# Optimization experiments

Measured on AMD Instinct MI355X. Metric: run time of the kernel, lower is better.

Reference implementation:

```python
import jax, jax.numpy as jnp
import numpy as np

B = 32768          # batch
M = 128            # m_spa, embedding dim
N_TAB = 26         # number of sparse tables
N_ROWS = 100000    # rows per table
LN_BOT = [13, 512, 256, 128]
LN_TOP = [479, 1024, 1024, 1]  # 479 = 128 + 27*26/2

# strictly-lower-triangle indices of the (1+N_TAB) x (1+N_TAB) interaction matrix,
# in the same row-major order as the torch list-comprehension.
_LI, _LJ = np.tril_indices(N_TAB + 1, k=-1)


def _mlp_params(key, ln):
    ws, bs = [], []
    for i in range(len(ln) - 1):
        n, m = ln[i], ln[i + 1]
        key, k1, k2 = jax.random.split(key, 3)
        ws.append(jax.random.normal(k1, (m, n), jnp.float32) * np.sqrt(2.0 / (m + n)))
        bs.append(jax.random.normal(k2, (m,), jnp.float32) * np.sqrt(1.0 / m))
    return ws, bs


def setup_inputs() -> dict:
    key = jax.random.key(0)
    kd, ki, ke, kb, kt = jax.random.split(key, 5)
    dense_x = jax.random.normal(kd, (B, LN_BOT[0]), jnp.float32)
    lS_i = jax.random.randint(ki, (N_TAB, B), 0, N_ROWS, dtype=jnp.int64)
    lS_o = jnp.tile(jnp.arange(B, dtype=jnp.int64), (N_TAB, 1))  # one index per bag
    bound = np.sqrt(1.0 / N_ROWS)
    emb_W = jax.random.uniform(ke, (N_TAB, N_ROWS, M), jnp.float32, -bound, bound)
    bw, bb = _mlp_params(kb, LN_BOT)
    tw, tb = _mlp_params(kt, LN_TOP)
    return {
        "dense_x": dense_x, "lS_i": lS_i, "lS_o": lS_o, "emb_W": emb_W,
        "bot_w0": bw[0], "bot_b0": bb[0], "bot_w1": bw[1], "bot_b1": bb[1],
        "bot_w2": bw[2], "bot_b2": bb[2],
        "top_w0": tw[0], "top_b0": tb[0], "top_w1": tw[1], "top_b1": tb[1],
        "top_w2": tw[2], "top_b2": tb[2],
    }


def _forward(dense_x, lS_i, emb_W,
             bot_w0, bot_b0, bot_w1, bot_b1, bot_w2, bot_b2,
             top_w0, top_b0, top_w1, top_b1, top_w2, top_b2):
    # bottom MLP (all ReLU, sigmoid_bot = -1)
    x = jax.nn.relu(dense_x @ bot_w0.T + bot_b0)
    x = jax.nn.relu(x @ bot_w1.T + bot_b1)
    x = jax.nn.relu(x @ bot_w2.T + bot_b2)                      # [B, M]
    # embedding lookups; offsets are arange(B) -> sum-pool of a single index == gather
    ly = jax.vmap(lambda W, idx: W[idx])(emb_W, lS_i)           # [N_TAB, B, M]
    # pairwise feature interaction
    T = jnp.concatenate([x[:, None, :], jnp.transpose(ly, (1, 0, 2))], axis=1)  # [B, 27, M]
    Z = jnp.einsum('bid,bjd->bij', T, T)                        # [B, 27, 27]
    Zflat = Z[:, _LI, _LJ]                                      # [B, 351]
    R = jnp.concatenate([x, Zflat], axis=1)                     # [B, 479]
    # top MLP (ReLU, ReLU, Sigmoid at layer index 2)
    z = jax.nn.relu(R @ top_w0.T + top_b0)
    z = jax.nn.relu(z @ top_w1.T + top_b1)
    p = jax.nn.sigmoid(z @ top_w2.T + top_b2)                   # [B, 1]
    return p  # loss_threshold == 0.0 -> no clamp


def reference(dense_x, lS_i, lS_o, emb_W,
              bot_w0, bot_b0, bot_w1, bot_b1, bot_w2, bot_b2,
              top_w0, top_b0, top_w1, top_b1, top_w2, top_b2):
    del lS_o  # offsets = arange(B): one index per bag, pooling is identity
    return _forward(dense_x, lS_i, emb_W,
                    bot_w0, bot_b0, bot_w1, bot_b1, bot_w2, bot_b2,
                    top_w0, top_b0, top_w1, top_b1, top_w2, top_b2)
```

## Files before the change

kernel.cpp:

```cpp
#include <hip/hip_runtime.h>

typedef unsigned short u16;
typedef unsigned int   u32;
typedef __attribute__((ext_vector_type(4))) float f32x4;
typedef __attribute__((ext_vector_type(8))) short bf16x8;

__device__ __forceinline__ u16 f2bf(float f) {
  u32 u = __float_as_uint(f);
  u = (u + 0x7FFFu + ((u >> 16) & 1u)) >> 16;
  return (u16)u;
}
__device__ __forceinline__ float bf2f(u16 h) {
  return __uint_as_float(((u32)h) << 16);
}

#define GLDS16(gptr, lptr)                                      \
  __builtin_amdgcn_global_load_lds(                             \
      (const __attribute__((address_space(1))) void*)(gptr),    \
      (__attribute__((address_space(3))) void*)(lptr), 16, 0, 0)

__global__ __launch_bounds__(256) void cvt_w(const float* __restrict__ src,
                                             u16* __restrict__ dst, int n) {
  int i = blockIdx.x * 256 + threadIdx.x;
  if (i < n) dst[i] = f2bf(src[i]);
}

__global__ __launch_bounds__(256) void cvt_w_pad(const float* __restrict__ src,
                                                 u16* __restrict__ dst,
                                                 int N, int Ksrc, int Kdst) {
  int i = blockIdx.x * 256 + threadIdx.x;
  if (i < N * Kdst) {
    int r = i / Kdst, k = i - r * Kdst;
    dst[i] = (k < Ksrc) ? f2bf(src[(size_t)r * Ksrc + k]) : (u16)0;
  }
}

__global__ __launch_bounds__(256) void bot0(const float* __restrict__ dense,
                                            const float* __restrict__ w0,
                                            const float* __restrict__ b0,
                                            u16* __restrict__ x1) {
  const int t = blockIdx.x * 256 + threadIdx.x;
  const int b = t >> 9, n = t & 511;
  const float* dr = dense + (size_t)b * 13;
  const float* wr = w0 + (size_t)n * 13;
  float s = b0[n];
#pragma unroll
  for (int k = 0; k < 13; ++k) s = fmaf(dr[k], wr[k], s);
  x1[t] = f2bf(fmaxf(s, 0.f));
}

__global__ __launch_bounds__(256) void gemm_bt_relu(
    const u16* __restrict__ A, const u16* __restrict__ W,
    const float* __restrict__ bias, u16* __restrict__ C,
    int M, int N, int K) {
  __shared__ u16 Al[128 * 32];
  __shared__ u16 Bl[128 * 32];
  const int tid = threadIdx.x;
  const int wave = tid >> 6, lane = tid & 63;
  const int ntn = N >> 7;
  const int bm = blockIdx.x / ntn, bn = blockIdx.x % ntn;
  const int wm = (wave >> 1) << 6, wn = (wave & 1) << 6;
  const int fr = lane & 15, fq = lane >> 4;

  const int srow = wave * 16 + (lane >> 2);
  const int scol = (lane & 3) * 8;
  const u16* ag0 = A + (size_t)(bm * 128 + srow) * K + scol;
  const u16* ag1 = ag0 + (size_t)64 * K;
  const u16* wg0 = W + (size_t)(bn * 128 + srow) * K + scol;
  const u16* wg1 = wg0 + (size_t)64 * K;
  u16* la0 = &Al[(wave * 16) * 32];
  u16* la1 = &Al[(64 + wave * 16) * 32];
  u16* lb0 = &Bl[(wave * 16) * 32];
  u16* lb1 = &Bl[(64 + wave * 16) * 32];

  f32x4 acc[4][4] = {};

  for (int kt = 0; kt < K; kt += 32) {
    __syncthreads();
    GLDS16(ag0 + kt, la0);
    GLDS16(ag1 + kt, la1);
    GLDS16(wg0 + kt, lb0);
    GLDS16(wg1 + kt, lb1);
    __syncthreads();
    bf16x8 af[4], bfv[4];
#pragma unroll
    for (int i = 0; i < 4; ++i) {
      af[i]  = *(const bf16x8*)&Al[(wm + i * 16 + fr) * 32 + fq * 8];
      bfv[i] = *(const bf16x8*)&Bl[(wn + i * 16 + fr) * 32 + fq * 8];
    }
#pragma unroll
    for (int i = 0; i < 4; ++i)
#pragma unroll
      for (int j = 0; j < 4; ++j)
        acc[i][j] = __builtin_amdgcn_mfma_f32_16x16x32_bf16(af[i], bfv[j],
                                                            acc[i][j], 0, 0, 0);
  }

  const int crow0 = bm * 128 + wm, ccol0 = bn * 128 + wn;
#pragma unroll
  for (int i = 0; i < 4; ++i) {
#pragma unroll
    for (int j = 0; j < 4; ++j) {
      const int col = ccol0 + j * 16 + fr;
      const float bv = bias[col];
#pragma unroll
      for (int rr = 0; rr < 4; ++rr) {
        const int row = crow0 + i * 16 + fq * 4 + rr;
        float v = acc[i][j][rr] + bv;
        v = fmaxf(v, 0.f);
        C[(size_t)row * N + col] = f2bf(v);
      }
    }
  }
}

__global__ __launch_bounds__(256) void interact(const float* __restrict__ emb,
                                                const int* __restrict__ lsi,
                                                const u16* __restrict__ x3,
                                                u16* __restrict__ R) {
  const int wave = threadIdx.x >> 6, lane = threadIdx.x & 63;
  const int b = blockIdx.x * 4 + wave;
  const int fr = lane & 15, fq = lane >> 4;
  const u16* x3b = x3 + (size_t)b * 128;
  u16* Rb = R + (size_t)b * 512;

  *(u32*)&Rb[lane * 2] = *(const u32*)&x3b[lane * 2];
  if (lane < 33) Rb[479 + lane] = 0;

  bf16x8 tf[2][4];
#pragma unroll
  for (int mi = 0; mi < 2; ++mi) {
    const int row = mi * 16 + fr;
    if (row == 0) {
#pragma unroll
      for (int ks = 0; ks < 4; ++ks)
        tf[mi][ks] = *(const bf16x8*)&x3b[ks * 32 + fq * 8];
    } else if (row <= 26) {
      const int idx = lsi[(size_t)(row - 1) * 32768 + b];
      const float* er = emb + ((size_t)(row - 1) * 100000 + (size_t)idx) * 128;
#pragma unroll
      for (int ks = 0; ks < 4; ++ks) {
        f32x4 u0 = *(const f32x4*)&er[ks * 32 + fq * 8];
        f32x4 u1 = *(const f32x4*)&er[ks * 32 + fq * 8 + 4];
        bf16x8 v;
#pragma unroll
        for (int j = 0; j < 4; ++j) {
          v[j] = (short)f2bf(u0[j]);
          v[j + 4] = (short)f2bf(u1[j]);
        }
        tf[mi][ks] = v;
      }
    } else {
      bf16x8 z = {0, 0, 0, 0, 0, 0, 0, 0};
#pragma unroll
      for (int ks = 0; ks < 4; ++ks) tf[mi][ks] = z;
    }
  }

  f32x4 acc[2][2] = {};
#pragma unroll
  for (int ks = 0; ks < 4; ++ks)
#pragma unroll
    for (int mi = 0; mi < 2; ++mi)
#pragma unroll
      for (int ni = 0; ni < 2; ++ni)
        acc[mi][ni] = __builtin_amdgcn_mfma_f32_16x16x32_bf16(
            tf[mi][ks], tf[ni][ks], acc[mi][ni], 0, 0, 0);

#pragma unroll
  for (int mi = 0; mi < 2; ++mi)
#pragma unroll
    for (int ni = 0; ni < 2; ++ni)
#pragma unroll
      for (int rr = 0; rr < 4; ++rr) {
        const int i = mi * 16 + fq * 4 + rr;
        const int j = ni * 16 + fr;
        if (i < 27 && j < i)
          Rb[128 + (i * (i - 1)) / 2 + j] = f2bf(acc[mi][ni][rr]);
      }
}

__global__ __launch_bounds__(256) void final_k(const u16* __restrict__ z2,
                                               const float* __restrict__ w,
                                               const float* __restrict__ b2,
                                               float* __restrict__ out) {
  const int wave = threadIdx.x >> 6, lane = threadIdx.x & 63;
  const int b = blockIdx.x * 4 + wave;
  const u16* zr = z2 + (size_t)b * 1024;
  bf16x8 v0 = *(const bf16x8*)&zr[lane * 16];
  bf16x8 v1 = *(const bf16x8*)&zr[lane * 16 + 8];
  float s = 0.f;
#pragma unroll
  for (int j = 0; j < 8; ++j) {
    s = fmaf(bf2f((u16)v0[j]), w[lane * 16 + j], s);
    s = fmaf(bf2f((u16)v1[j]), w[lane * 16 + 8 + j], s);
  }
#pragma unroll
  for (int off = 32; off > 0; off >>= 1) s += __shfl_down(s, off, 64);
  if (lane == 0) out[b] = 1.f / (1.f + expf(-(s + b2[0])));
}

extern "C" void kernel_launch(void* const* d_in, const int* in_sizes, int n_in,
                              void* d_out, int out_size, void* d_ws,
                              size_t ws_size, hipStream_t stream) {
  const float* dense = (const float*)d_in[0];
  const int*   lsi   = (const int*)d_in[1];
  const float* emb = (const float*)d_in[3];
  const float* bw0 = (const float*)d_in[4];
  const float* bb0 = (const float*)d_in[5];
  const float* bw1 = (const float*)d_in[6];
  const float* bb1 = (const float*)d_in[7];
  const float* bw2 = (const float*)d_in[8];
  const float* bb2 = (const float*)d_in[9];
  const float* tw0 = (const float*)d_in[10];
  const float* tb0 = (const float*)d_in[11];
  const float* tw1 = (const float*)d_in[12];
  const float* tb1 = (const float*)d_in[13];
  const float* tw2 = (const float*)d_in[14];
  const float* tb2 = (const float*)d_in[15];

  char* ws = (char*)d_ws;
  u16* W1B  = (u16*)ws; ws += (size_t)256 * 512 * 2;
  u16* W2B  = (u16*)ws; ws += (size_t)128 * 256 * 2;
  u16* TW0B = (u16*)ws; ws += (size_t)1024 * 512 * 2;
  u16* TW1B = (u16*)ws; ws += (size_t)1024 * 1024 * 2;
  u16* X3   = (u16*)ws; ws += (size_t)32768 * 128 * 2;
  u16* SA   = (u16*)ws; ws += (size_t)32768 * 1024 * 2;
  u16* SB   = (u16*)ws; ws += (size_t)32768 * 1024 * 2;

  cvt_w<<<512, 256, 0, stream>>>(bw1, W1B, 256 * 512);
  cvt_w<<<128, 256, 0, stream>>>(bw2, W2B, 128 * 256);
  cvt_w_pad<<<2048, 256, 0, stream>>>(tw0, TW0B, 1024, 479, 512);
  cvt_w<<<4096, 256, 0, stream>>>(tw1, TW1B, 1024 * 1024);

  bot0<<<65536, 256, 0, stream>>>(dense, bw0, bb0, SA);
  gemm_bt_relu<<<512, 256, 0, stream>>>(SA, W1B, bb1, SB, 32768, 256, 512);
  gemm_bt_relu<<<256, 256, 0, stream>>>(SB, W2B, bb2, X3, 32768, 128, 256);
  interact<<<8192, 256, 0, stream>>>(emb, lsi, X3, SA);
  gemm_bt_relu<<<2048, 256, 0, stream>>>(SA, TW0B, tb0, SB, 32768, 1024, 512);
  gemm_bt_relu<<<2048, 256, 0, stream>>>(SB, TW1B, tb1, SA, 32768, 1024, 1024);
  final_k<<<8192, 256, 0, stream>>>(SA, tw2, tb2, (float*)d_out);
}
```

Measured before the change: 381.0 us.

## Add pipelined 256x256 GEMM for top MLP and fuse final dot into epilogue

Replaces the two large top-MLP GEMMs with a new 512-thread 256x256-tile kernel. It double-buffers LDS tiles via direct global-to-LDS loads, interleaves MFMA quarters with staged loads, raises wave priority around the MFMA blocks, and uses an XCD-aware block swizzle. The last GEMM's epilogue now computes the final 1024->1 dot product through atomicAdd into a float buffer, followed by a small sigmoid kernel. This removes the write and re-read of the 32768x1024 bf16 activation, at the cost of atomics, a zeroing kernel and a non-deterministic summation order.

```diff
diff --git a/kernel.cpp b/kernel.cpp
--- a/kernel.cpp
+++ b/kernel.cpp
@@ -18,6 +18,18 @@
   __builtin_amdgcn_global_load_lds(                             \
       (const __attribute__((address_space(1))) void*)(gptr),    \
       (__attribute__((address_space(3))) void*)(lptr), 16, 0, 0)
+
+#define BARRIER                                                 \
+  do {                                                          \
+    asm volatile("" ::: "memory");                              \
+    __builtin_amdgcn_s_barrier();                               \
+    asm volatile("" ::: "memory");                              \
+  } while (0)
+#define WAITLGKM0 asm volatile("s_waitcnt lgkmcnt(0)" ::: "memory")
+#define WAITVM2   asm volatile("s_waitcnt vmcnt(2)" ::: "memory")
+#define WAITVM0   asm volatile("s_waitcnt vmcnt(0)" ::: "memory")
+#define PRIO1 __builtin_amdgcn_s_setprio(1)
+#define PRIO0 __builtin_amdgcn_s_setprio(0)
 
 __global__ __launch_bounds__(256) void cvt_w(const float* __restrict__ src,
                                              u16* __restrict__ dst, int n) {
@@ -114,6 +126,139 @@
   }
 }
 
+#define LDA4(dst, FB, BUFE)                                                    \
+  _Pragma("unroll") for (int f = 0; f < 4; ++f)                                \
+  _Pragma("unroll") for (int ks = 0; ks < 2; ++ks)                             \
+    dst[f][ks] = *(const bf16x8*)&lds[(BUFE) +                                 \
+        (wm * 128 + (FB) * 16 + f * 16 + fr) * 64 +                            \
+        ((ks * 4 + fq) ^ fr7) * 8];
+
+#define LDB2(dst, GB, BUFE)                                                    \
+  _Pragma("unroll") for (int g = 0; g < 2; ++g)                                \
+  _Pragma("unroll") for (int ks = 0; ks < 2; ++ks)                             \
+    dst[g][ks] = *(const bf16x8*)&lds[(BUFE) + 16384 +                         \
+        (wn * 64 + (GB) * 16 + g * 16 + fr) * 64 +                             \
+        ((ks * 4 + fq) ^ fr7) * 8];
+
+#define MFQ(FB, GB, va, vb)                                                    \
+  _Pragma("unroll") for (int f = 0; f < 4; ++f)                                \
+  _Pragma("unroll") for (int g = 0; g < 2; ++g)                                \
+  _Pragma("unroll") for (int ks = 0; ks < 2; ++ks)                             \
+    acc[(FB) + f][(GB) + g] = __builtin_amdgcn_mfma_f32_16x16x32_bf16(         \
+        va[f][ks], vb[g][ks], acc[(FB) + f][(GB) + g], 0, 0, 0);
+
+template <int FUSE>
+__global__ __launch_bounds__(512, 2) void gemm256(
+    const u16* __restrict__ Ap, const u16* __restrict__ Wp,
+    const float* __restrict__ bias, u16* __restrict__ C,
+    const float* __restrict__ w2, float* __restrict__ dotacc,
+    int N, int K) {
+  __shared__ u16 lds[65536];
+  const int tid = threadIdx.x;
+  const int wave = tid >> 6, lane = tid & 63;
+  const int wm = wave >> 2, wn = wave & 3;
+  const int fr = lane & 15, fq = lane >> 4, fr7 = fr & 7;
+  const int nkt = K >> 6, NP = nkt >> 1;
+
+  const int nwg = gridDim.x;
+  const int swz = (blockIdx.x & 7) * (nwg >> 3) + (blockIdx.x >> 3);
+  const int ntn = N >> 8;
+  const int bm = swz / ntn, bn = swz % ntn;
+
+  auto stageH = [&](int tile, int half) {
+    const int isB = half >> 1;
+    const int h128 = half & 1;
+    const u16* mat = isB ? Wp : Ap;
+    const int brow0 = (isB ? bn : bm) * 256 + h128 * 128;
+    u16* lb = lds + (tile & 1) * 32768 + isB * 16384 + h128 * 8192 + wave * 512;
+    const int sl = lane >> 3;
+    const int ch = (lane & 7) ^ sl;
+    const u16* g = mat + (size_t)(brow0 + wave * 8 + sl) * K + tile * 64 + ch * 8;
+    GLDS16(g, lb);
+    GLDS16(g + (size_t)64 * K, lb + 4096);
+  };
+
+  f32x4 acc[8][4] = {};
+
+  stageH(0, 0); stageH(0, 1); stageH(0, 2); stageH(0, 3);
+  stageH(1, 0);
+  WAITVM2;
+  BARRIER;
+
+  for (int p = 0; p < NP; ++p) {
+    const int todd = 2 * p + 1, t2 = 2 * p + 2, t3 = 2 * p + 3;
+    const bool last = (p == NP - 1);
+    bf16x8 va[4][2], vb0[2][2], vb1[2][2];
+
+    LDA4(va, 0, 0); LDB2(vb0, 0, 0);
+    stageH(todd, 1);
+    BARRIER; WAITLGKM0; PRIO1; MFQ(0, 0, va, vb0); PRIO0; BARRIER;
+    LDB2(vb1, 2, 0);
+    stageH(todd, 2);
+    BARRIER; WAITLGKM0; PRIO1; MFQ(0, 2, va, vb1); PRIO0; BARRIER;
+    LDA4(va, 4, 0);
+    stageH(todd, 3);
+    BARRIER; WAITLGKM0; PRIO1; MFQ(4, 0, va, vb0); PRIO0; BARRIER;
+    if (t2 < nkt) stageH(t2, 0);
+    BARRIER; PRIO1; MFQ(4, 2, va, vb1); PRIO0;
+    if (last) { WAITVM0; } else { WAITVM2; }
+    BARRIER;
+
+    LDA4(va, 0, 32768); LDB2(vb0, 0, 32768);
+    if (t2 < nkt) stageH(t2, 1);
+    BARRIER; WAITLGKM0; PRIO1; MFQ(0, 0, va, vb0); PRIO0; BARRIER;
+    LDB2(vb1, 2, 32768);
+    if (t2 < nkt) stageH(t2, 2);
+    BARRIER; WAITLGKM0; PRIO1; MFQ(0, 2, va, vb1); PRIO0; BARRIER;
+    LDA4(va, 4, 32768);
+    if (t2 < nkt) stageH(t2, 3);
+    BARRIER; WAITLGKM0; PRIO1; MFQ(4, 0, va, vb0); PRIO0; BARRIER;
+    if (t3 < nkt) stageH(t3, 0);
+    BARRIER; PRIO1; MFQ(4, 2, va, vb1); PRIO0;
+    if (!last) { WAITVM2; }
+    BARRIER;
+  }
+
+  const int r0 = bm * 256 + wm * 128;
+  const int c0 = bn * 256 + wn * 64;
+  if (FUSE) {
+    float bv[4], wv[4];
+#pragma unroll
+    for (int g = 0; g < 4; ++g) {
+      const int col = c0 + g * 16 + fr;
+      bv[g] = bias[col];
+      wv[g] = w2[col];
+    }
+#pragma unroll
+    for (int f = 0; f < 8; ++f) {
+#pragma unroll
+      for (int rr = 0; rr < 4; ++rr) {
+        float s = 0.f;
+#pragma unroll
+        for (int g = 0; g < 4; ++g)
+          s += fmaxf(acc[f][g][rr] + bv[g], 0.f) * wv[g];
+#pragma unroll
+        for (int off = 8; off >= 1; off >>= 1) s += __shfl_xor(s, off, 64);
+        if (fr == 0)
+          atomicAdd(&dotacc[r0 + f * 16 + fq * 4 + rr], s);
+      }
+    }
+  } else {
+#pragma unroll
+    for (int g = 0; g < 4; ++g) {
+      const int col = c0 + g * 16 + fr;
+      const float bvv = bias[col];
+#pragma unroll
+      for (int f = 0; f < 8; ++f)
+#pragma unroll
+        for (int rr = 0; rr < 4; ++rr) {
+          const int row = r0 + f * 16 + fq * 4 + rr;
+          C[(size_t)row * N + col] = f2bf(fmaxf(acc[f][g][rr] + bvv, 0.f));
+        }
+    }
+  }
+}
+
 __global__ __launch_bounds__(256) void interact(const float* __restrict__ emb,
                                                 const int* __restrict__ lsi,
                                                 const u16* __restrict__ x3,
@@ -180,24 +325,16 @@
       }
 }
 
-__global__ __launch_bounds__(256) void final_k(const u16* __restrict__ z2,
-                                               const float* __restrict__ w,
-                                               const float* __restrict__ b2,
-                                               float* __restrict__ out) {
-  const int wave = threadIdx.x >> 6, lane = threadIdx.x & 63;
-  const int b = blockIdx.x * 4 + wave;
-  const u16* zr = z2 + (size_t)b * 1024;
-  bf16x8 v0 = *(const bf16x8*)&zr[lane * 16];
-  bf16x8 v1 = *(const bf16x8*)&zr[lane * 16 + 8];
-  float s = 0.f;
-#pragma unroll
-  for (int j = 0; j < 8; ++j) {
-    s = fmaf(bf2f((u16)v0[j]), w[lane * 16 + j], s);
-    s = fmaf(bf2f((u16)v1[j]), w[lane * 16 + 8 + j], s);
-  }
-#pragma unroll
-  for (int off = 32; off > 0; off >>= 1) s += __shfl_down(s, off, 64);
-  if (lane == 0) out[b] = 1.f / (1.f + expf(-(s + b2[0])));
+__global__ __launch_bounds__(256) void zero_f(float* __restrict__ p, int n) {
+  int i = blockIdx.x * 256 + threadIdx.x;
+  if (i < n) p[i] = 0.f;
+}
+
+__global__ __launch_bounds__(256) void sig_k(const float* __restrict__ accv,
+                                             const float* __restrict__ b2,
+                                             float* __restrict__ out, int n) {
+  int i = blockIdx.x * 256 + threadIdx.x;
+  if (i < n) out[i] = 1.f / (1.f + expf(-(accv[i] + b2[0])));
 }
 
 extern "C" void kernel_launch(void* const* d_in, const int* in_sizes, int n_in,
@@ -224,6 +361,7 @@
   u16* W2B  = (u16*)ws; ws += (size_t)128 * 256 * 2;
   u16* TW0B = (u16*)ws; ws += (size_t)1024 * 512 * 2;
   u16* TW1B = (u16*)ws; ws += (size_t)1024 * 1024 * 2;
+  float* DOT = (float*)ws; ws += (size_t)32768 * 4;
   u16* X3   = (u16*)ws; ws += (size_t)32768 * 128 * 2;
   u16* SA   = (u16*)ws; ws += (size_t)32768 * 1024 * 2;
   u16* SB   = (u16*)ws; ws += (size_t)32768 * 1024 * 2;
@@ -232,12 +370,15 @@
   cvt_w<<<128, 256, 0, stream>>>(bw2, W2B, 128 * 256);
   cvt_w_pad<<<2048, 256, 0, stream>>>(tw0, TW0B, 1024, 479, 512);
   cvt_w<<<4096, 256, 0, stream>>>(tw1, TW1B, 1024 * 1024);
+  zero_f<<<128, 256, 0, stream>>>(DOT, 32768);
 
   bot0<<<65536, 256, 0, stream>>>(dense, bw0, bb0, SA);
   gemm_bt_relu<<<512, 256, 0, stream>>>(SA, W1B, bb1, SB, 32768, 256, 512);
   gemm_bt_relu<<<256, 256, 0, stream>>>(SB, W2B, bb2, X3, 32768, 128, 256);
   interact<<<8192, 256, 0, stream>>>(emb, lsi, X3, SA);
-  gemm_bt_relu<<<2048, 256, 0, stream>>>(SA, TW0B, tb0, SB, 32768, 1024, 512);
-  gemm_bt_relu<<<2048, 256, 0, stream>>>(SB, TW1B, tb1, SA, 32768, 1024, 1024);
-  final_k<<<8192, 256, 0, stream>>>(SA, tw2, tb2, (float*)d_out);
-}
+  gemm256<0><<<512, 512, 0, stream>>>(SA, TW0B, tb0, SB, nullptr, nullptr,
+                                      1024, 512);
+  gemm256<1><<<512, 512, 0, stream>>>(SB, TW1B, tb1, nullptr, tw2, DOT,
+                                      1024, 1024);
+  sig_k<<<128, 256, 0, stream>>>(DOT, tb2, (float*)d_out, 32768);
+}
```

Result: faster. 335.2 us (-12.0%).
